# Kernel tuning notes

Hardware: AMD Instinct MI355X
Metric: run time of the kernel (lower is better)

Reference implementation:

```python
import jax, jax.numpy as jnp
import numpy as np

EMBED = 512
HEADS = 8
HD = EMBED // HEADS  # 64
NCLS = 1
WSIZE = 32
DIL = 2
WIN_LEN = 2 * WSIZE + 1  # 65


def setup_inputs() -> dict:
    key = jax.random.key(0)
    ks = jax.random.split(key, 5)
    B, S = 2, NCLS + 2048
    return {
        "x": jax.random.normal(ks[0], (B, S, EMBED), dtype=jnp.float32),
        "qkv_w": jax.random.normal(ks[1], (3 * EMBED, EMBED), dtype=jnp.float32) * 0.02,
        "qkv_b": jax.random.normal(ks[2], (3 * EMBED,), dtype=jnp.float32) * 0.02,
        "out_w": jax.random.normal(ks[3], (EMBED, EMBED), dtype=jnp.float32) * 0.02,
        "out_b": jax.random.normal(ks[4], (EMBED,), dtype=jnp.float32) * 0.02,
    }


def reference(x, qkv_w, qkv_b, out_w, out_b):
    B, S, E = x.shape
    P = S - NCLS  # patch_len
    scale = HD ** -0.5

    qkv = (x @ qkv_w.T + qkv_b).reshape(B, S, 3, HEADS, HD)
    qkv = qkv.transpose(2, 0, 3, 1, 4)  # (3, B, H, S, d)
    q, k, v = qkv[0], qkv[1], qkv[2]

    q_cls, k_cls, v_cls = q[:, :, :NCLS], k[:, :, :NCLS], v[:, :, :NCLS]
    q_p, k_p, v_p = q[:, :, NCLS:], k[:, :, NCLS:], v[:, :, NCLS:]

    # CLS queries: full attention over all S keys
    s_cls = jnp.einsum('bhqd,bhkd->bhqk', q_cls, k) * scale
    cls_out = jnp.einsum('bhqk,bhkd->bhqd', jax.nn.softmax(s_cls, axis=-1), v)

    # Patch queries: CLS keys + dilated local window
    pad = WSIZE * DIL
    kp = jnp.pad(k_p, ((0, 0), (0, 0), (pad, pad), (0, 0)))
    vp = jnp.pad(v_p, ((0, 0), (0, 0), (pad, pad), (0, 0)))
    idx = jnp.arange(P)[:, None] + jnp.arange(WIN_LEN)[None, :] * DIL  # (P, WL)
    kw = kp[:, :, idx]  # (B, H, P, WL, d)
    vw = vp[:, :, idx]

    sw = jnp.einsum('bhpd,bhpwd->bhpw', q_p, kw) * scale
    pos = jnp.arange(P)[:, None] + (jnp.arange(WIN_LEN) - WSIZE)[None, :] * DIL
    in_bounds = (pos >= 0) & (pos < P)  # (P, WL)
    sw = jnp.where(in_bounds[None, None], sw, -jnp.inf)
    sc = jnp.einsum('bhpd,bhcd->bhpc', q_p, k_cls) * scale

    attn = jax.nn.softmax(jnp.concatenate([sc, sw], axis=-1), axis=-1)
    a_c, a_w = attn[..., :NCLS], attn[..., NCLS:]
    patch_out = (jnp.einsum('bhpc,bhcd->bhpd', a_c, v_cls)
                 + jnp.einsum('bhpw,bhpwd->bhpd', a_w, vw))

    out = jnp.concatenate([cls_out, patch_out], axis=2)  # (B, H, S, d)
    out = out.transpose(0, 2, 1, 3).reshape(B, S, E)
    return out @ out_w.T + out_b
```

## Files before the change

kernel.cpp:

```cpp
#include <hip/hip_runtime.h>
#include <math.h>

#define S_LEN 2049
#define P_LEN 2048
#define EMB 512
#define NH 8
#define HD 64
#define SCALE 0.125f

typedef _Float16 f16x8 __attribute__((ext_vector_type(8)));
typedef float f32x4 __attribute__((ext_vector_type(4)));
typedef unsigned short u16x8 __attribute__((ext_vector_type(8)));

__device__ inline unsigned short f2h(float f) {
  _Float16 h = (_Float16)f;
  return __builtin_bit_cast(unsigned short, h);
}
__device__ inline float h2f(unsigned short u) {
  return (float)__builtin_bit_cast(_Float16, u);
}

__device__ inline float wave_sum64(float v) {
#pragma unroll
  for (int off = 32; off > 0; off >>= 1) v += __shfl_xor(v, off, 64);
  return v;
}

__device__ inline void gld16(const unsigned* g, unsigned* l) {
  __builtin_amdgcn_global_load_lds(
      (const __attribute__((address_space(1))) unsigned*)g,
      (__attribute__((address_space(3))) unsigned*)l, 16, 0, 0);
}

__global__ __launch_bounds__(256) void cvt3_f16(
    const float* __restrict__ s0, unsigned short* __restrict__ d0, int n0,
    const float* __restrict__ s1, unsigned short* __restrict__ d1, int n1,
    const float* __restrict__ s2, unsigned short* __restrict__ d2, int n2) {
  int idx = (blockIdx.x * 256 + threadIdx.x) * 8;
  const float* s;
  unsigned short* d;
  int off;
  if (idx < n0) {
    s = s0; d = d0; off = idx;
  } else if (idx < n0 + n1) {
    s = s1; d = d1; off = idx - n0;
  } else if (idx < n0 + n1 + n2) {
    s = s2; d = d2; off = idx - n0 - n1;
  } else {
    return;
  }
  float4 f0 = *(const float4*)(s + off);
  float4 f1 = *(const float4*)(s + off + 4);
  float ff[8] = {f0.x, f0.y, f0.z, f0.w, f1.x, f1.y, f1.z, f1.w};
  u16x8 vh;
#pragma unroll
  for (int e = 0; e < 8; e++) vh[e] = f2h(ff[e]);
  *(u16x8*)(d + off) = vh;
}

template <int BM, int BN, bool F16OUT>
__global__ __launch_bounds__(256) void gemm_f16(
    const unsigned short* __restrict__ A, const unsigned short* __restrict__ B,
    const float* __restrict__ bias, void* __restrict__ Cv, int M, int N,
    int KP) {
  constexpr int BK = 64;
  __shared__ __align__(16) unsigned short As[BM * BK];
  __shared__ __align__(16) unsigned short Bs[BN * BK];
  const int t = threadIdx.x;
  const int lane = t & 63, wv = t >> 6;
  const int m0 = blockIdx.x * BM, n0 = blockIdx.y * BN;
  constexpr int WM = BM / 2, WN = BN / 2;
  constexpr int RM = WM / 16, RN = WN / 16;
  const int wm = wv & 1, wn = wv >> 1;
  const int lm = lane & 15, lq = lane >> 4;

  f32x4 acc[RM][RN];
#pragma unroll
  for (int i = 0; i < RM; i++)
#pragma unroll
    for (int j = 0; j < RN; j++) acc[i][j] = (f32x4){0.f, 0.f, 0.f, 0.f};

  const int lr = lane >> 3;
  const int lc = (lane & 7) ^ lr;

  const unsigned* aptr[BM / 32];
#pragma unroll
  for (int p = 0; p < BM / 32; p++) {
    int ra = wv * (BM / 4) + p * 8 + lr;
    int gr = m0 + ra;
    gr = gr < M ? gr : M - 1;
    aptr[p] = (const unsigned*)(A + (size_t)gr * KP + lc * 8);
  }
  const unsigned* bptr[BN / 32];
#pragma unroll
  for (int p = 0; p < BN / 32; p++) {
    int rb = wv * (BN / 4) + p * 8 + lr;
    bptr[p] = (const unsigned*)(B + (size_t)(n0 + rb) * KP + lc * 8);
  }

  for (int kt = 0; kt < KP; kt += BK) {
    __syncthreads();
#pragma unroll
    for (int p = 0; p < BM / 32; p++)
      gld16(aptr[p] + (kt >> 1), (unsigned*)&As[(wv * (BM / 4) + p * 8) * BK]);
#pragma unroll
    for (int p = 0; p < BN / 32; p++)
      gld16(bptr[p] + (kt >> 1), (unsigned*)&Bs[(wv * (BN / 4) + p * 8) * BK]);
    __syncthreads();

    f16x8 fa[2][RM], fb[2][RN];
#pragma unroll
    for (int kk = 0; kk < 2; kk++) {
      int ch = ((kk * 4 + lq) ^ (lm & 7)) * 8;
#pragma unroll
      for (int mi = 0; mi < RM; mi++) {
        int ra = wm * WM + mi * 16 + lm;
        fa[kk][mi] = *(const f16x8*)&As[ra * BK + ch];
      }
#pragma unroll
      for (int ni = 0; ni < RN; ni++) {
        int rb = wn * WN + ni * 16 + lm;
        fb[kk][ni] = *(const f16x8*)&Bs[rb * BK + ch];
      }
    }
#pragma unroll
    for (int kk = 0; kk < 2; kk++)
#pragma unroll
      for (int mi = 0; mi < RM; mi++)
#pragma unroll
        for (int ni = 0; ni < RN; ni++)
          acc[mi][ni] = __builtin_amdgcn_mfma_f32_16x16x32_f16(
              fa[kk][mi], fb[kk][ni], acc[mi][ni], 0, 0, 0);
  }

#pragma unroll
  for (int ni = 0; ni < RN; ni++) {
    int n = n0 + wn * WN + ni * 16 + lm;
    float bv = bias[n];
#pragma unroll
    for (int mi = 0; mi < RM; mi++)
#pragma unroll
      for (int r = 0; r < 4; r++) {
        int m = m0 + wm * WM + mi * 16 + lq * 4 + r;
        if (m < M) {
          float val = acc[mi][ni][r] + bv;
          if constexpr (F16OUT)
            ((unsigned short*)Cv)[(size_t)m * N + n] = f2h(val);
          else
            ((float*)Cv)[(size_t)m * N + n] = val;
        }
      }
  }
}

__global__ __launch_bounds__(256) void patch_attn3(
    const unsigned short* __restrict__ qkv16,
    unsigned short* __restrict__ Aatt) {
  constexpr int LDK = 72;
  constexpr int LDT = 168;
  __shared__ __align__(16) unsigned short Ks[144 * LDK];
  __shared__ __align__(16) unsigned short Vt[64 * LDT];
  __shared__ __align__(16) unsigned short Ps[64 * LDT];

  const int t = threadIdx.x;
  const int lane = t & 63, wv = t >> 6;
  const int lm = lane & 15, lq = lane >> 4;
  const int qb = blockIdx.x;
  const int h = blockIdx.y;
  const int par = blockIdx.z & 1, b = blockIdx.z >> 1;
  const unsigned short* base = qkv16 + (size_t)b * S_LEN * 1536;
  const int qc0 = qb * 64;

  {
    uint4 z = {0, 0, 0, 0};
    for (int i = t; i < 144 * LDK / 8; i += 256) ((uint4*)Ks)[i] = z;
    for (int i = t; i < 64 * LDT / 8; i += 256) ((uint4*)Vt)[i] = z;
    for (int i = t; i < 64 * LDT / 8; i += 256) ((uint4*)Ps)[i] = z;
  }
  __syncthreads();

  {
    int rr = t >> 4;
    int cc = (t & 15) * 4;
#pragma unroll
    for (int pass = 0; pass < 8; pass++) {
      int r = pass * 16 + rr;
      int jc = qc0 - 32 + r;
      uint2 kv = {0, 0};
      if ((unsigned)jc < 1024u)
        kv = *(const uint2*)(base + (size_t)(1 + 2 * jc + par) * 1536 + 512 +
                             h * 64 + cc);
      *(uint2*)&Ks[r * LDK + cc] = kv;
    }
    if (rr == 0)
      *(uint2*)&Ks[128 * LDK + cc] =
          *(const uint2*)(base + 512 + h * 64 + cc);
  }
#pragma unroll
  for (int pass = 0; pass < 4; pass++) {
    int task = pass * 256 + t;
    int jp = task >> 4;
    int d0 = (task & 15) * 4;
    int jc0 = qc0 - 32 + 2 * jp;
    uint2 a = {0, 0}, c = {0, 0};
    if ((unsigned)jc0 < 1024u)
      a = *(const uint2*)(base + (size_t)(1 + 2 * jc0 + par) * 1536 + 1024 +
                          h * 64 + d0);
    if ((unsigned)(jc0 + 1) < 1024u)
      c = *(const uint2*)(base + (size_t)(1 + 2 * (jc0 + 1) + par) * 1536 +
                          1024 + h * 64 + d0);
    *(unsigned*)&Vt[(d0 + 0) * LDT + 2 * jp] = (a.x & 0xffffu) | (c.x << 16);
    *(unsigned*)&Vt[(d0 + 1) * LDT + 2 * jp] = (a.x >> 16) | (c.x & 0xffff0000u);
    *(unsigned*)&Vt[(d0 + 2) * LDT + 2 * jp] = (a.y & 0xffffu) | (c.y << 16);
    *(unsigned*)&Vt[(d0 + 3) * LDT + 2 * jp] = (a.y >> 16) | (c.y & 0xffff0000u);
  }
  if (t < 64) Vt[t * LDT + 128] = base[1024 + h * 64 + t];

  const int qi = wv * 16 + lm;
  const unsigned short* qg =
      base + (size_t)(1 + 2 * (qc0 + qi) + par) * 1536 + h * 64;
  f16x8 qf[2];
  qf[0] = *(const f16x8*)&qg[lq * 8];
  qf[1] = *(const f16x8*)&qg[32 + lq * 8];
  __syncthreads();

  f32x4 s[9];
#pragma unroll
  for (int nt = 0; nt < 9; nt++) s[nt] = (f32x4){0.f, 0.f, 0.f, 0.f};
#pragma unroll
  for (int nt = 0; nt < 9; nt++) {
#pragma unroll
    for (int kk = 0; kk < 2; kk++) {
      f16x8 kb = *(const f16x8*)&Ks[(nt * 16 + lm) * LDK + kk * 32 + lq * 8];
      s[nt] =
          __builtin_amdgcn_mfma_f32_16x16x32_f16(qf[kk], kb, s[nt], 0, 0, 0);
    }
  }

  float L[4];
#pragma unroll
  for (int r = 0; r < 4; r++) {
    int qrow = wv * 16 + lq * 4 + r;
    float sv[9];
    float mx = -1e30f;
#pragma unroll
    for (int nt = 0; nt < 9; nt++) {
      int jl = nt * 16 + lm;
      bool valid =
          (jl == 128) ||
          (jl < 128 && jl >= qrow && jl <= qrow + 64 &&
           (unsigned)(qc0 - 32 + jl) < 1024u);
      sv[nt] = valid ? s[nt][r] * SCALE : -1e30f;
      mx = fmaxf(mx, sv[nt]);
    }
#pragma unroll
    for (int off = 1; off < 16; off <<= 1)
      mx = fmaxf(mx, __shfl_xor(mx, off, 16));
    float l = 0.f;
#pragma unroll
    for (int nt = 0; nt < 9; nt++) {
      float e = __expf(sv[nt] - mx);
      l += e;
      Ps[qrow * LDT + nt * 16 + lm] = f2h(e);
    }
#pragma unroll
    for (int off = 1; off < 16; off <<= 1) l += __shfl_xor(l, off, 16);
    L[r] = l;
  }
  __syncthreads();

  f32x4 oa[4];
#pragma unroll
  for (int nt = 0; nt < 4; nt++) oa[nt] = (f32x4){0.f, 0.f, 0.f, 0.f};
#pragma unroll
  for (int kc = 0; kc < 5; kc++) {
    f16x8 pa = *(const f16x8*)&Ps[(wv * 16 + lm) * LDT + kc * 32 + lq * 8];
#pragma unroll
    for (int nt = 0; nt < 4; nt++) {
      f16x8 vb = *(const f16x8*)&Vt[(nt * 16 + lm) * LDT + kc * 32 + lq * 8];
      oa[nt] = __builtin_amdgcn_mfma_f32_16x16x32_f16(pa, vb, oa[nt], 0, 0, 0);
    }
  }

#pragma unroll
  for (int r = 0; r < 4; r++) {
    float inv = 1.f / L[r];
    int qrow = wv * 16 + lq * 4 + r;
    int pp = 2 * (qc0 + qrow) + par;
    unsigned short* ab = Aatt + ((size_t)b * S_LEN + 1 + pp) * 512 + h * 64;
#pragma unroll
    for (int nt = 0; nt < 4; nt++) ab[nt * 16 + lm] = f2h(oa[nt][r] * inv);
  }
}

__global__ __launch_bounds__(256) void cls_part_k(
    const unsigned short* __restrict__ qkv16, float* __restrict__ Pm,
    float* __restrict__ Pl, float* __restrict__ Po) {
  const int lane = threadIdx.x & 63;
  const int wv = threadIdx.x >> 6;
  const int ck = blockIdx.x;
  const int h = blockIdx.y;
  const int b = blockIdx.z;
  const unsigned short* base = qkv16 + (size_t)b * S_LEN * 1536;
  float qd = h2f(base[h * 64 + lane]) * SCALE;

  int c0 = ck * 64;
  int cend = (ck == 31) ? S_LEN : c0 + 64;

  float m = -1e30f, l = 0.f, o = 0.f;
  for (int j = c0 + wv; j < cend; j += 4) {
    const unsigned short* krow = base + (size_t)j * 1536 + 512 + h * 64;
    float kv = h2f(krow[lane]);
    float vv = h2f(krow[512 + lane]);
    float s = wave_sum64(qd * kv);
    float mn = fmaxf(m, s);
    float e0 = __expf(m - mn);
    float e1 = __expf(s - mn);
    l = l * e0 + e1;
    o = o * e0 + e1 * vv;
    m = mn;
  }

  __shared__ float sm[4], sl[4], so[4][64];
  if (lane == 0) {
    sm[wv] = m;
    sl[wv] = l;
  }
  so[wv][lane] = o;
  __syncthreads();
  if (wv == 0) {
    float M = -1e30f;
#pragma unroll
    for (int i = 0; i < 4; i++) M = fmaxf(M, sm[i]);
    float L = 0.f, O = 0.f;
#pragma unroll
    for (int i = 0; i < 4; i++) {
      float c = __expf(sm[i] - M);
      L += sl[i] * c;
      O += so[i][lane] * c;
    }
    int idx = (b * NH + h) * 32 + ck;
    if (lane == 0) {
      Pm[idx] = M;
      Pl[idx] = L;
    }
    Po[(size_t)idx * 64 + lane] = O;
  }
}

__global__ __launch_bounds__(64) void cls_comb_k(
    const float* __restrict__ Pm, const float* __restrict__ Pl,
    const float* __restrict__ Po, unsigned short* __restrict__ Aatt) {
  const int lane = threadIdx.x;
  const int h = blockIdx.x % NH;
  const int b = blockIdx.x / NH;
  float m = -1e30f, l = 0.f, o = 0.f;
  for (int ck = 0; ck < 32; ck++) {
    int idx = (b * NH + h) * 32 + ck;
    float mc = Pm[idx];
    float lc = Pl[idx];
    float oc = Po[(size_t)idx * 64 + lane];
    float mn = fmaxf(m, mc);
    float e0 = __expf(m - mn);
    float e1 = __expf(mc - mn);
    l = l * e0 + lc * e1;
    o = o * e0 + oc * e1;
    m = mn;
  }
  Aatt[(size_t)b * S_LEN * 512 + h * HD + lane] = f2h(o / l);
}

extern "C" void kernel_launch(void* const* d_in, const int* in_sizes, int n_in,
                              void* d_out, int out_size, void* d_ws,
                              size_t ws_size, hipStream_t stream) {
  const float* x = (const float*)d_in[0];
  const float* qkv_w = (const float*)d_in[1];
  const float* qkv_b = (const float*)d_in[2];
  const float* out_w = (const float*)d_in[3];
  const float* out_b = (const float*)d_in[4];
  float* out = (float*)d_out;

  const int M = 2 * S_LEN;

  float* cls_pm = (float*)d_ws;
  float* cls_pl = cls_pm + 512;
  float* cls_po = cls_pl + 512;
  unsigned short* Xp = (unsigned short*)(cls_po + 32768);
  unsigned short* Wq = Xp + (size_t)M * 512;
  unsigned short* Wo = Wq + (size_t)1536 * 512;
  unsigned short* Aatt = Wo + (size_t)512 * 512;
  unsigned short* qkv16 = Aatt + (size_t)M * 512;

  const int n0 = M * EMB;
  const int n1 = 1536 * EMB;
  const int n2 = EMB * EMB;
  int cvt_blocks = ((n0 + n1 + n2) / 8 + 255) / 256;
  cvt3_f16<<<cvt_blocks, 256, 0, stream>>>(x, Xp, n0, qkv_w, Wq, n1, out_w, Wo,
                                           n2);

  dim3 gq((M + 63) / 64, 1536 / 128);
  gemm_f16<64, 128, true><<<gq, 256, 0, stream>>>(Xp, Wq, qkv_b, qkv16, M,
                                                  1536, 512);

  cls_part_k<<<dim3(32, NH, 2), 256, 0, stream>>>(qkv16, cls_pm, cls_pl,
                                                  cls_po);
  cls_comb_k<<<2 * NH, 64, 0, stream>>>(cls_pm, cls_pl, cls_po, Aatt);
  patch_attn3<<<dim3(16, NH, 4), 256, 0, stream>>>(qkv16, Aatt);

  dim3 go((M + 63) / 64, EMB / 64);
  gemm_f16<64, 64, false><<<go, 256, 0, stream>>>(Aatt, Wo, out_b, out, M, EMB,
                                                  512);
}
```

Before: 122.2 us.

## Fuse CLS combine into patch attention, widen GEMM K-tile, trim LDS zeroing

```diff
diff --git a/kernel.cpp b/kernel.cpp
--- a/kernel.cpp
+++ b/kernel.cpp
@@ -63,7 +63,7 @@
     const unsigned short* __restrict__ A, const unsigned short* __restrict__ B,
     const float* __restrict__ bias, void* __restrict__ Cv, int M, int N,
     int KP) {
-  constexpr int BK = 64;
+  constexpr int BK = 128;
   __shared__ __align__(16) unsigned short As[BM * BK];
   __shared__ __align__(16) unsigned short Bs[BN * BK];
   const int t = threadIdx.x;
@@ -80,57 +80,57 @@
 #pragma unroll
     for (int j = 0; j < RN; j++) acc[i][j] = (f32x4){0.f, 0.f, 0.f, 0.f};
 
-  const int lr = lane >> 3;
-  const int lc = (lane & 7) ^ lr;
-
-  const unsigned* aptr[BM / 32];
-#pragma unroll
-  for (int p = 0; p < BM / 32; p++) {
-    int ra = wv * (BM / 4) + p * 8 + lr;
-    int gr = m0 + ra;
+  const int lr4 = lane >> 4;
+  const int pos = lane & 15;
+
+  const unsigned* aptr[BM / 16];
+#pragma unroll
+  for (int p = 0; p < BM / 16; p++) {
+    int row = wv * (BM / 4) + p * 4 + lr4;
+    int sc = pos ^ (row & 15);
+    int gr = m0 + row;
     gr = gr < M ? gr : M - 1;
-    aptr[p] = (const unsigned*)(A + (size_t)gr * KP + lc * 8);
-  }
-  const unsigned* bptr[BN / 32];
-#pragma unroll
-  for (int p = 0; p < BN / 32; p++) {
-    int rb = wv * (BN / 4) + p * 8 + lr;
-    bptr[p] = (const unsigned*)(B + (size_t)(n0 + rb) * KP + lc * 8);
+    aptr[p] = (const unsigned*)(A + (size_t)gr * KP + sc * 8);
+  }
+  const unsigned* bptr[BN / 16];
+#pragma unroll
+  for (int p = 0; p < BN / 16; p++) {
+    int rb = wv * (BN / 4) + p * 4 + lr4;
+    int sc = pos ^ (rb & 15);
+    bptr[p] = (const unsigned*)(B + (size_t)(n0 + rb) * KP + sc * 8);
   }
 
   for (int kt = 0; kt < KP; kt += BK) {
     __syncthreads();
 #pragma unroll
-    for (int p = 0; p < BM / 32; p++)
-      gld16(aptr[p] + (kt >> 1), (unsigned*)&As[(wv * (BM / 4) + p * 8) * BK]);
-#pragma unroll
-    for (int p = 0; p < BN / 32; p++)
-      gld16(bptr[p] + (kt >> 1), (unsigned*)&Bs[(wv * (BN / 4) + p * 8) * BK]);
+    for (int p = 0; p < BM / 16; p++)
+      gld16(aptr[p] + (kt >> 1), (unsigned*)&As[(wv * (BM / 4) + p * 4) * BK]);
+#pragma unroll
+    for (int p = 0; p < BN / 16; p++)
+      gld16(bptr[p] + (kt >> 1), (unsigned*)&Bs[(wv * (BN / 4) + p * 4) * BK]);
     __syncthreads();
 
-    f16x8 fa[2][RM], fb[2][RN];
-#pragma unroll
-    for (int kk = 0; kk < 2; kk++) {
-      int ch = ((kk * 4 + lq) ^ (lm & 7)) * 8;
+#pragma unroll
+    for (int kk = 0; kk < 4; kk++) {
+      int posc = ((kk * 4 + lq) ^ lm) * 8;
+      f16x8 fa[RM], fb[RN];
 #pragma unroll
       for (int mi = 0; mi < RM; mi++) {
         int ra = wm * WM + mi * 16 + lm;
-        fa[kk][mi] = *(const f16x8*)&As[ra * BK + ch];
+        fa[mi] = *(const f16x8*)&As[ra * BK + posc];
       }
 #pragma unroll
       for (int ni = 0; ni < RN; ni++) {
         int rb = wn * WN + ni * 16 + lm;
-        fb[kk][ni] = *(const f16x8*)&Bs[rb * BK + ch];
+        fb[ni] = *(const f16x8*)&Bs[rb * BK + posc];
       }
-    }
-#pragma unroll
-    for (int kk = 0; kk < 2; kk++)
 #pragma unroll
       for (int mi = 0; mi < RM; mi++)
 #pragma unroll
         for (int ni = 0; ni < RN; ni++)
           acc[mi][ni] = __builtin_amdgcn_mfma_f32_16x16x32_f16(
-              fa[kk][mi], fb[kk][ni], acc[mi][ni], 0, 0, 0);
+              fa[mi], fb[ni], acc[mi][ni], 0, 0, 0);
+    }
   }
 
 #pragma unroll
@@ -154,8 +154,9 @@
 }
 
 __global__ __launch_bounds__(256) void patch_attn3(
-    const unsigned short* __restrict__ qkv16,
-    unsigned short* __restrict__ Aatt) {
+    const unsigned short* __restrict__ qkv16, unsigned short* __restrict__ Aatt,
+    const float* __restrict__ Pm, const float* __restrict__ Pl,
+    const float* __restrict__ Po) {
   constexpr int LDK = 72;
   constexpr int LDT = 168;
   __shared__ __align__(16) unsigned short Ks[144 * LDK];
@@ -163,19 +164,49 @@
   __shared__ __align__(16) unsigned short Ps[64 * LDT];
 
   const int t = threadIdx.x;
-  const int lane = t & 63, wv = t >> 6;
-  const int lm = lane & 15, lq = lane >> 4;
   const int qb = blockIdx.x;
   const int h = blockIdx.y;
   const int par = blockIdx.z & 1, b = blockIdx.z >> 1;
+
+  if (qb == 16) {
+    if (par == 0 && t < 64) {
+      float m = -1e30f, l = 0.f, o = 0.f;
+      for (int ck = 0; ck < 32; ck++) {
+        int idx = (b * NH + h) * 32 + ck;
+        float mc = Pm[idx];
+        float lc = Pl[idx];
+        float oc = Po[(size_t)idx * 64 + t];
+        float mn = fmaxf(m, mc);
+        float e0 = __expf(m - mn);
+        float e1 = __expf(mc - mn);
+        l = l * e0 + lc * e1;
+        o = o * e0 + oc * e1;
+        m = mn;
+      }
+      Aatt[(size_t)b * S_LEN * 512 + h * HD + t] = f2h(o / l);
+    }
+    return;
+  }
+
+  const int lane = t & 63, wv = t >> 6;
+  const int lm = lane & 15, lq = lane >> 4;
   const unsigned short* base = qkv16 + (size_t)b * S_LEN * 1536;
   const int qc0 = qb * 64;
 
   {
     uint4 z = {0, 0, 0, 0};
-    for (int i = t; i < 144 * LDK / 8; i += 256) ((uint4*)Ks)[i] = z;
-    for (int i = t; i < 64 * LDT / 8; i += 256) ((uint4*)Vt)[i] = z;
-    for (int i = t; i < 64 * LDT / 8; i += 256) ((uint4*)Ps)[i] = z;
+    if (t < 135) {
+      int row = 129 + t / 9, q = t % 9;
+      *(uint4*)&Ks[row * LDK + q * 8] = z;
+    }
+    {
+      int row = t >> 2, q = t & 3;
+      *(uint4*)&Vt[row * LDT + 128 + q * 8] = z;
+    }
+    if (t < 128) {
+      int row = t >> 1, q = t & 1;
+      *(uint4*)&Ps[row * LDT + 144 + q * 8] = z;
+    }
   }
   __syncthreads();
 
@@ -193,8 +224,7 @@
       *(uint2*)&Ks[r * LDK + cc] = kv;
     }
     if (rr == 0)
-      *(uint2*)&Ks[128 * LDK + cc] =
-          *(const uint2*)(base + 512 + h * 64 + cc);
+      *(uint2*)&Ks[128 * LDK + cc] = *(const uint2*)(base + 512 + h * 64 + cc);
   }
 #pragma unroll
   for (int pass = 0; pass < 4; pass++) {
@@ -348,28 +378,6 @@
   }
 }
 
-__global__ __launch_bounds__(64) void cls_comb_k(
-    const float* __restrict__ Pm, const float* __restrict__ Pl,
-    const float* __restrict__ Po, unsigned short* __restrict__ Aatt) {
-  const int lane = threadIdx.x;
-  const int h = blockIdx.x % NH;
-  const int b = blockIdx.x / NH;
-  float m = -1e30f, l = 0.f, o = 0.f;
-  for (int ck = 0; ck < 32; ck++) {
-    int idx = (b * NH + h) * 32 + ck;
-    float mc = Pm[idx];
-    float lc = Pl[idx];
-    float oc = Po[(size_t)idx * 64 + lane];
-    float mn = fmaxf(m, mc);
-    float e0 = __expf(m - mn);
-    float e1 = __expf(mc - mn);
-    l = l * e0 + lc * e1;
-    o = o * e0 + oc * e1;
-    m = mn;
-  }
-  Aatt[(size_t)b * S_LEN * 512 + h * HD + lane] = f2h(o / l);
-}
-
 extern "C" void kernel_launch(void* const* d_in, const int* in_sizes, int n_in,
                               void* d_out, int out_size, void* d_ws,
                               size_t ws_size, hipStream_t stream) {
@@ -404,8 +412,8 @@
 
   cls_part_k<<<dim3(32, NH, 2), 256, 0, stream>>>(qkv16, cls_pm, cls_pl,
                                                   cls_po);
-  cls_comb_k<<<2 * NH, 64, 0, stream>>>(cls_pm, cls_pl, cls_po, Aatt);
-  patch_attn3<<<dim3(16, NH, 4), 256, 0, stream>>>(qkv16, Aatt);
+  patch_attn3<<<dim3(17, NH, 4), 256, 0, stream>>>(qkv16, Aatt, cls_pm, cls_pl,
+                                                   cls_po);
 
   dim3 go((M + 63) / 64, EMB / 64);
   gemm_f16<64, 64, false><<<go, 256, 0, stream>>>(Aatt, Wo, out_b, out, M, EMB,
```

After: 128.2 us. 4.9% more time.
